# Performance work log

Hardware: AMD Instinct MI355X
Metric: run time of the kernel (lower is better)

Reference implementation:

```python
import jax, jax.numpy as jnp
import numpy as np

MASK_DENSITY = 0.1  # fraction of nonzero weights kept by the sparsity mask


def setup_inputs() -> dict:
    key = jax.random.key(0)
    k_data, k_w, k_m, k_b = jax.random.split(key, 4)
    tokens, in_f, out_f = 8192, 4096, 4096
    data = jax.random.normal(k_data, (tokens, in_f), dtype=jnp.float32)
    weight = jax.random.normal(k_w, (out_f, in_f), dtype=jnp.float32)
    mask = (jax.random.uniform(k_m, (out_f, in_f)) < MASK_DENSITY).astype(jnp.float32)
    bias = jax.random.normal(k_b, (out_f,), dtype=jnp.float32)
    return {"data": data, "weight": weight, "mask": mask, "bias": bias}


def reference(data, weight, mask, bias):
    # out = data @ (mask * weight)^T + bias  (sparse linear; CSR of mask*weight
    # in the original kernel -- dense math is identical).
    w_sp = mask * weight                      # [out_f, in_f]
    out = jnp.einsum("ti,oi->to", data, w_sp) # [tokens, out_f]
    return out + bias
```

## Files before the change

### kernel.cpp

```cpp
#include <hip/hip_runtime.h>
#include <hip/hip_bf16.h>


#define GM 8192
#define GN 4096
#define GK 4096
#define NT (GK / 32)

typedef __attribute__((ext_vector_type(8))) short short8;
typedef __attribute__((ext_vector_type(8))) short bf16x8;
typedef __attribute__((ext_vector_type(4))) float f32x4;

__device__ __forceinline__ short f2bf(float x) {
    unsigned u = __builtin_bit_cast(unsigned, x);
    u += 0x7fffu + ((u >> 16) & 1u);
    return (short)(u >> 16);
}

__device__ __forceinline__ void stage16(const short* g, short* l) {
    __builtin_amdgcn_global_load_lds(
        (const __attribute__((address_space(1))) unsigned int*)g,
        (__attribute__((address_space(3))) unsigned int*)l, 16, 0, 0);
}

__global__ void cvt_data_kernel(const float* __restrict__ in, short* __restrict__ out, long n) {
    long i0 = ((long)blockIdx.x * blockDim.x + threadIdx.x) * 8;
    long stride = (long)gridDim.x * blockDim.x * 8;
    for (long i = i0; i < n; i += stride) {
        float4 a = *(const float4*)(in + i);
        float4 b = *(const float4*)(in + i + 4);
        short8 o;
        o[0] = f2bf(a.x); o[1] = f2bf(a.y); o[2] = f2bf(a.z); o[3] = f2bf(a.w);
        o[4] = f2bf(b.x); o[5] = f2bf(b.y); o[6] = f2bf(b.z); o[7] = f2bf(b.w);
        *(short8*)(out + i) = o;
    }
}

__global__ void cvt_w_kernel(const float* __restrict__ w, const float* __restrict__ m,
                             short* __restrict__ out, long n) {
    long i0 = ((long)blockIdx.x * blockDim.x + threadIdx.x) * 8;
    long stride = (long)gridDim.x * blockDim.x * 8;
    for (long i = i0; i < n; i += stride) {
        float4 wa = *(const float4*)(w + i);
        float4 wb = *(const float4*)(w + i + 4);
        float4 ma = *(const float4*)(m + i);
        float4 mb = *(const float4*)(m + i + 4);
        short8 o;
        o[0] = f2bf(wa.x * ma.x); o[1] = f2bf(wa.y * ma.y);
        o[2] = f2bf(wa.z * ma.z); o[3] = f2bf(wa.w * ma.w);
        o[4] = f2bf(wb.x * mb.x); o[5] = f2bf(wb.y * mb.y);
        o[6] = f2bf(wb.z * mb.z); o[7] = f2bf(wb.w * mb.w);
        *(short8*)(out + i) = o;
    }
}

__global__ __launch_bounds__(512, 4) void gemm_tlp(const short* __restrict__ A,
                                                   const short* __restrict__ B,
                                                   const float* __restrict__ bias,
                                                   float* __restrict__ C) {
    __shared__ short lds[36864];

    const int tid  = threadIdx.x;
    const int lane = tid & 63;
    const int wid  = tid >> 6;
    const int wr   = wid >> 1;
    const int wc   = wid & 1;

    const int bid  = blockIdx.x;
    const int swz  = (bid & 7) * 128 + (bid >> 3);
    const int brow = (swz >> 5) << 8;
    const int bcol = (swz & 31) << 7;

    const int trow = tid >> 2;
    const int qlog = (tid & 3) ^ ((((trow >> 3) & 1) << 1) | ((trow >> 1) & 1));

    const int l15 = lane & 15;
    const int q   = lane >> 4;
    const int qx  = (((l15 >> 3) & 1) << 1) | ((l15 >> 1) & 1);
    const int foff = l15 * 32 + ((q ^ qx) << 3);
    const int aOff = wr * 2048 + foff;
    const int bOff = 8192 + wc * 2048 + foff;

    f32x4 acc[4][4] = {};

    auto stageAB = [&](int sb, size_t kcol) {
        #pragma unroll
        for (int j = 0; j < 2; ++j)
            stage16(A + (size_t)(brow + j * 128 + trow) * GK + kcol + qlog * 8,
                    &lds[sb + j * 4096 + wid * 512]);
        stage16(B + (size_t)(bcol + trow) * GK + kcol + qlog * 8,
                &lds[sb + 8192 + wid * 512]);
    };

    stageAB(0, 0);
    stageAB(12288, 32);
    asm volatile("s_waitcnt vmcnt(3)" ::: "memory");
    __builtin_amdgcn_s_barrier();
    asm volatile("" ::: "memory");

    int cur = 0, st2 = 2;
    for (int T = 0; T < NT; ++T) {
        const int cb = cur * 12288;
        const bool stg = (T + 2 < NT);
        if (stg) stageAB(st2 * 12288, (size_t)(T + 2) * 32);

        bf16x8 af[4], bf[4];
        #pragma unroll
        for (int m = 0; m < 4; ++m) af[m] = *(const bf16x8*)&lds[cb + aOff + m * 512];
        #pragma unroll
        for (int n = 0; n < 4; ++n) bf[n] = *(const bf16x8*)&lds[cb + bOff + n * 512];

        __builtin_amdgcn_s_setprio(1);
        #pragma unroll
        for (int m = 0; m < 4; ++m)
            #pragma unroll
            for (int n = 0; n < 4; ++n)
                acc[m][n] = __builtin_amdgcn_mfma_f32_16x16x32_bf16(af[m], bf[n], acc[m][n], 0, 0, 0);
        __builtin_amdgcn_s_setprio(0);

        if (stg)                { asm volatile("s_waitcnt vmcnt(3)" ::: "memory"); }
        else if (T + 2 == NT)   { asm volatile("s_waitcnt vmcnt(0)" ::: "memory"); }
        __builtin_amdgcn_s_barrier();
        asm volatile("" ::: "memory");

        if (++cur == 3) cur = 0;
        if (++st2 == 3) st2 = 0;
    }

    #pragma unroll
    for (int n = 0; n < 4; ++n) {
        const int col = bcol + wc * 64 + n * 16 + l15;
        const float bv = bias[col];
        #pragma unroll
        for (int m = 0; m < 4; ++m) {
            const int rowb = brow + wr * 64 + m * 16 + (q << 2);
            #pragma unroll
            for (int r = 0; r < 4; ++r)
                C[(size_t)(rowb + r) * GN + col] = acc[m][n][r] + bv;
        }
    }
}

extern "C" void kernel_launch(void* const* d_in, const int* in_sizes, int n_in,
                              void* d_out, int out_size, void* d_ws, size_t ws_size,
                              hipStream_t stream) {
    const float* data   = (const float*)d_in[0];
    const float* weight = (const float*)d_in[1];
    const float* mask   = (const float*)d_in[2];
    const float* bias   = (const float*)d_in[3];
    float* out = (float*)d_out;

    short* dataB = (short*)d_ws;
    short* wB    = dataB + (size_t)GM * GK;

    cvt_data_kernel<<<2048, 256, 0, stream>>>(data, dataB, (long)GM * GK);
    cvt_w_kernel<<<2048, 256, 0, stream>>>(weight, mask, wB, (long)GN * GK);

    gemm_tlp<<<1024, 512, 0, stream>>>(dataB, wB, bias, out);
}
```

Baseline: 348.3 us.

## Switch GEMM to 256x256 tiles with 4 waves and register double-buffered fragments

The GEMM now uses 256-thread blocks, each computing a 256x256 output tile, with every wave holding a 128x128 sub-tile (8x8 MFMA accumulators). LDS fragments for the next k-step are loaded into a second register set while the current MFMAs run, and the loop is manually unrolled by two. The aim is to raise arithmetic intensity per LDS/global byte and hide LDS latency behind MFMA work. In exchange, register pressure rises sharply (256 accumulator floats plus 32 fragment vectors), occupancy drops to one block per CU, and there are only 512 blocks for the device's CUs.

```diff
diff --git a/kernel.cpp b/kernel.cpp
--- a/kernel.cpp
+++ b/kernel.cpp
@@ -54,11 +54,11 @@
     }
 }
 
-__global__ __launch_bounds__(512, 4) void gemm_tlp(const short* __restrict__ A,
-                                                   const short* __restrict__ B,
-                                                   const float* __restrict__ bias,
-                                                   float* __restrict__ C) {
-    __shared__ short lds[36864];
+__global__ __launch_bounds__(256, 1) void gemm_4w(const short* __restrict__ A,
+                                                  const short* __restrict__ B,
+                                                  const float* __restrict__ bias,
+                                                  float* __restrict__ C) {
+    __shared__ short lds[49152];
 
     const int tid  = threadIdx.x;
     const int lane = tid & 63;
@@ -67,9 +67,9 @@
     const int wc   = wid & 1;
 
     const int bid  = blockIdx.x;
-    const int swz  = (bid & 7) * 128 + (bid >> 3);
-    const int brow = (swz >> 5) << 8;
-    const int bcol = (swz & 31) << 7;
+    const int swz  = (bid & 7) * 64 + (bid >> 3);
+    const int brow = (swz >> 4) << 8;
+    const int bcol = (swz & 15) << 8;
 
     const int trow = tid >> 2;
     const int qlog = (tid & 3) ^ ((((trow >> 3) & 1) << 1) | ((trow >> 1) & 1));
@@ -78,62 +78,70 @@
     const int q   = lane >> 4;
     const int qx  = (((l15 >> 3) & 1) << 1) | ((l15 >> 1) & 1);
     const int foff = l15 * 32 + ((q ^ qx) << 3);
-    const int aOff = wr * 2048 + foff;
-    const int bOff = 8192 + wc * 2048 + foff;
+    const int aOff = wr * 4096 + foff;
+    const int bOff = 8192 + wc * 4096 + foff;
 
-    f32x4 acc[4][4] = {};
+    f32x4 acc[8][8] = {};
+    bf16x8 afA[8], bfA[8], afB[8], bfB[8];
 
-    auto stageAB = [&](int sb, size_t kcol) {
+    auto stage = [&](int sb, size_t kcol) {
         #pragma unroll
-        for (int j = 0; j < 2; ++j)
-            stage16(A + (size_t)(brow + j * 128 + trow) * GK + kcol + qlog * 8,
-                    &lds[sb + j * 4096 + wid * 512]);
-        stage16(B + (size_t)(bcol + trow) * GK + kcol + qlog * 8,
-                &lds[sb + 8192 + wid * 512]);
+        for (int j = 0; j < 4; ++j)
+            stage16(A + (size_t)(brow + j * 64 + trow) * GK + kcol + qlog * 8,
+                    &lds[sb + j * 2048 + wid * 512]);
+        #pragma unroll
+        for (int j = 0; j < 4; ++j)
+            stage16(B + (size_t)(bcol + j * 64 + trow) * GK + kcol + qlog * 8,
+                    &lds[sb + 8192 + j * 2048 + wid * 512]);
     };
 
-    stageAB(0, 0);
-    stageAB(12288, 32);
-    asm volatile("s_waitcnt vmcnt(3)" ::: "memory");
+    stage(0, 0);
+    stage(16384, 32);
+    asm volatile("s_waitcnt vmcnt(8)" ::: "memory");
     __builtin_amdgcn_s_barrier();
     asm volatile("" ::: "memory");
+    #pragma unroll
+    for (int m = 0; m < 8; ++m) afA[m] = *(const bf16x8*)&lds[aOff + m * 512];
+    #pragma unroll
+    for (int n = 0; n < 8; ++n) bfA[n] = *(const bf16x8*)&lds[bOff + n * 512];
 
-    int cur = 0, st2 = 2;
-    for (int T = 0; T < NT; ++T) {
-        const int cb = cur * 12288;
-        const bool stg = (T + 2 < NT);
-        if (stg) stageAB(st2 * 12288, (size_t)(T + 2) * 32);
+#define BODY(T, CA, CB, NA, NB)                                                    \
+  {                                                                                 \
+    const bool stg = (T) + 2 < NT;                                                  \
+    if (stg) stage((((T) + 2) % 3) * 16384, (size_t)((T) + 2) * 32);                \
+    if (stg) { asm volatile("s_waitcnt vmcnt(8)" ::: "memory"); }                   \
+    else     { asm volatile("s_waitcnt vmcnt(0)" ::: "memory"); }                   \
+    __builtin_amdgcn_s_barrier();                                                   \
+    asm volatile("" ::: "memory");                                                  \
+    if ((T) + 1 < NT) {                                                             \
+      const int ns = (((T) + 1) % 3) * 16384;                                       \
+      _Pragma("unroll")                                                             \
+      for (int m = 0; m < 8; ++m) NA[m] = *(const bf16x8*)&lds[ns + aOff + m * 512];\
+      _Pragma("unroll")                                                             \
+      for (int n = 0; n < 8; ++n) NB[n] = *(const bf16x8*)&lds[ns + bOff + n * 512];\
+    }                                                                               \
+    __builtin_amdgcn_sched_barrier(0);                                              \
+    _Pragma("unroll")                                                               \
+    for (int m = 0; m < 8; ++m)                                                     \
+      _Pragma("unroll")                                                             \
+      for (int n = 0; n < 8; ++n)                                                   \
+        acc[m][n] = __builtin_amdgcn_mfma_f32_16x16x32_bf16(CA[m], CB[n],           \
+                                                            acc[m][n], 0, 0, 0);    \
+  }
 
-        bf16x8 af[4], bf[4];
-        #pragma unroll
-        for (int m = 0; m < 4; ++m) af[m] = *(const bf16x8*)&lds[cb + aOff + m * 512];
-        #pragma unroll
-        for (int n = 0; n < 4; ++n) bf[n] = *(const bf16x8*)&lds[cb + bOff + n * 512];
-
-        __builtin_amdgcn_s_setprio(1);
-        #pragma unroll
-        for (int m = 0; m < 4; ++m)
-            #pragma unroll
-            for (int n = 0; n < 4; ++n)
-                acc[m][n] = __builtin_amdgcn_mfma_f32_16x16x32_bf16(af[m], bf[n], acc[m][n], 0, 0, 0);
-        __builtin_amdgcn_s_setprio(0);
-
-        if (stg)                { asm volatile("s_waitcnt vmcnt(3)" ::: "memory"); }
-        else if (T + 2 == NT)   { asm volatile("s_waitcnt vmcnt(0)" ::: "memory"); }
-        __builtin_amdgcn_s_barrier();
-        asm volatile("" ::: "memory");
-
-        if (++cur == 3) cur = 0;
-        if (++st2 == 3) st2 = 0;
+    for (int T = 0; T < NT; T += 2) {
+        BODY(T,     afA, bfA, afB, bfB)
+        BODY(T + 1, afB, bfB, afA, bfA)
     }
+#undef BODY
 
     #pragma unroll
-    for (int n = 0; n < 4; ++n) {
-        const int col = bcol + wc * 64 + n * 16 + l15;
+    for (int n = 0; n < 8; ++n) {
+        const int col = bcol + wc * 128 + n * 16 + l15;
         const float bv = bias[col];
         #pragma unroll
-        for (int m = 0; m < 4; ++m) {
-            const int rowb = brow + wr * 64 + m * 16 + (q << 2);
+        for (int m = 0; m < 8; ++m) {
+            const int rowb = brow + wr * 128 + m * 16 + (q << 2);
             #pragma unroll
             for (int r = 0; r < 4; ++r)
                 C[(size_t)(rowb + r) * GN + col] = acc[m][n][r] + bv;
@@ -156,5 +164,5 @@
     cvt_data_kernel<<<2048, 256, 0, stream>>>(data, dataB, (long)GM * GK);
     cvt_w_kernel<<<2048, 256, 0, stream>>>(weight, mask, wB, (long)GN * GK);
 
-    gemm_tlp<<<1024, 512, 0, stream>>>(dataB, wB, bias, out);
+    gemm_4w<<<512, 256, 0, stream>>>(dataB, wB, bias, out);
 }
```

Result: slower. 830.0 us (+138.3%).
